# Kernel tuning notes

Measured on AMD Instinct MI355X. Metric: run time of the kernel, lower is better.

Reference implementation:

```python
import jax, jax.numpy as jnp
import numpy as np

ALPHA = 0.01  # leaky relu slope

def setup_inputs() -> dict:
    key = jax.random.key(0)
    ks = jax.random.split(key, 6)
    B, N1, N2, D_IN, D_OUT = 8, 2048, 2048, 256, 256
    return {
        "input_tensor1": jax.random.normal(ks[0], (B, N1, D_IN), jnp.float32),
        "attention_mask1": jnp.zeros((B, 1, N1), jnp.float32),
        "input_tensor2": jax.random.normal(ks[1], (B, N2, D_IN), jnp.float32),
        "attention_mask2": jnp.zeros((B, 1, N2), jnp.float32),
        "W1": jax.random.normal(ks[2], (D_IN, D_OUT), jnp.float32) * 0.05,
        "a1": jax.random.normal(ks[3], (2 * D_OUT, 1), jnp.float32) * 0.05,
        "W2": jax.random.normal(ks[4], (D_IN, D_OUT), jnp.float32) * 0.05,
        "a2": jax.random.normal(ks[5], (2 * D_OUT, 1), jnp.float32) * 0.05,
    }

def _cross_attn(Wh_q, Wh_k, a, mask):
    d = Wh_q.shape[-1]
    # additive GAT-style scores: [B, Nq, 1] + [B, 1, Nk] -> [B, Nq, Nk]
    s_q = Wh_q @ a[:d, :]            # [B, Nq, 1]
    s_k = Wh_k @ a[d:, :]            # [B, Nk, 1]
    e = s_q + jnp.swapaxes(s_k, -1, -2)
    e = jax.nn.leaky_relu(e, negative_slope=ALPHA)
    probs = jax.nn.softmax(e + mask, axis=-1)
    ctx = probs @ Wh_k               # [B, Nq, d]
    return ctx, probs

def reference(input_tensor1, attention_mask1, input_tensor2, attention_mask2, W1, a1, W2, a2):
    # dropout in eval mode (identity) for a deterministic reference
    Wh11 = input_tensor1 @ W1
    Wh12 = input_tensor2 @ W1
    ctx1, probs1 = _cross_attn(Wh11, Wh12, a1, attention_mask2)
    Wh22 = input_tensor2 @ W2
    Wh21 = input_tensor1 @ W2
    ctx2, probs2 = _cross_attn(Wh22, Wh21, a2, attention_mask1)
    return ctx1, ctx2, probs1, probs2
```

## Files before the change

kernel.cpp:

```cpp
#include <hip/hip_runtime.h>
#include <hip/hip_bf16.h>
#include <stdint.h>

#define ALPHA 0.01f

typedef __attribute__((ext_vector_type(8))) short short8;
typedef __attribute__((ext_vector_type(4))) float f32x4;
typedef __attribute__((ext_vector_type(4))) float float4_;
typedef __attribute__((ext_vector_type(4))) unsigned short ushort4_;
typedef unsigned int u32;

static __device__ __forceinline__ unsigned short f2bf(float f) {
    union { float f; u32 u; } v; v.f = f;
    u32 r = v.u + 0x7FFF + ((v.u >> 16) & 1);
    return (unsigned short)(r >> 16);
}

static __device__ __forceinline__ void lds_load16(const void* g, void* l) {
    __builtin_amdgcn_global_load_lds((const __attribute__((address_space(1))) u32*)g,
                                     (__attribute__((address_space(3))) u32*)l, 16, 0, 0);
}

__global__ __launch_bounds__(256) void k_prep(const float* __restrict__ W1, const float* __restrict__ a1,
                                              const float* __restrict__ W2, const float* __restrict__ a2,
                                              unsigned short* __restrict__ W1T, unsigned short* __restrict__ W2T,
                                              float* __restrict__ u) {
    int bb = blockIdx.x;
    if (bb < 512) {
        const float* W = (bb & 256) ? W2 : W1;
        unsigned short* WT = (bb & 256) ? W2T : W1T;
        int n = bb & 255, k = threadIdx.x;
        WT[n * 256 + k] = f2bf(W[k * 256 + n]);
    } else {
        int v = bb - 512;
        const float* W = (v < 2) ? W1 : W2;
        const float* a = ((v < 2) ? a1 : a2) + (v & 1) * 256;
        int d = threadIdx.x;
        float acc = 0.f;
        for (int n = 0; n < 256; n++) acc += W[d * 256 + n] * a[n];
        u[v * 256 + d] = acc;
    }
}

__global__ __launch_bounds__(256) void k_cast_s(const float* __restrict__ in1, const float* __restrict__ in2,
                                                const float* __restrict__ u,
                                                unsigned short* __restrict__ in1b, unsigned short* __restrict__ in2b,
                                                float* __restrict__ s) {
    int gid = blockIdx.x * 4 + (threadIdx.x >> 6);
    int tensor = gid >> 14;
    int row = gid & 16383;
    int lane = threadIdx.x & 63;
    const float* in = tensor ? in2 : in1;
    unsigned short* outb = tensor ? in2b : in1b;
    const float* uA = u + (tensor ? 256 : 0);
    const float* uB = u + (tensor ? 512 : 768);
    float* sA = s + (tensor ? 1 : 0) * 16384;
    float* sB = s + (tensor ? 2 : 3) * 16384;

    float4_ v = *(const float4_*)(in + row * 256 + lane * 4);
    float4_ ua = *(const float4_*)(uA + lane * 4);
    float4_ ub = *(const float4_*)(uB + lane * 4);
    ushort4_ ob;
    ob.x = f2bf(v.x); ob.y = f2bf(v.y); ob.z = f2bf(v.z); ob.w = f2bf(v.w);
    *(ushort4_*)(outb + row * 256 + lane * 4) = ob;
    float accA = v.x * ua.x + v.y * ua.y + v.z * ua.z + v.w * ua.w;
    float accB = v.x * ub.x + v.y * ub.y + v.z * ub.z + v.w * ub.w;
    for (int off = 32; off; off >>= 1) {
        accA += __shfl_xor(accA, off, 64);
        accB += __shfl_xor(accB, off, 64);
    }
    if (lane == 0) { sA[row] = accA; sB[row] = accB; }
}

__global__ __launch_bounds__(256) void k_gemm_whT(const unsigned short* __restrict__ W1T,
                                                  const unsigned short* __restrict__ W2T,
                                                  const unsigned short* __restrict__ in1b,
                                                  const unsigned short* __restrict__ in2b,
                                                  unsigned short* __restrict__ whT1,
                                                  unsigned short* __restrict__ whT2) {
    __shared__ __attribute__((aligned(16))) unsigned short sA[2][128 * 32];
    __shared__ __attribute__((aligned(16))) unsigned short sB[2][128 * 32];
    int c = blockIdx.x >> 8;
    int bid = blockIdx.x & 255;
    int mt = bid & 1, ntile = bid >> 1;
    const unsigned short* A = c ? W2T : W1T;
    const unsigned short* Bm = c ? in1b : in2b;
    unsigned short* outp = c ? whT2 : whT1;
    int t = threadIdx.x;
    int w = t >> 6, lane = t & 63, l15 = lane & 15, lq = lane >> 4;
    int wm = (w & 1) * 64, wn = (w >> 1) * 64;
    f32x4 acc[4][4] = {};
    const unsigned short* gA = A + (mt * 128 + (t >> 2)) * 256 + (t & 3) * 8;
    const unsigned short* gB = Bm + (ntile * 128 + (t >> 2)) * 256 + (t & 3) * 8;

    lds_load16(gA, &sA[0][t * 8]);
    lds_load16(gA + 64 * 256, &sA[0][t * 8 + 2048]);
    lds_load16(gB, &sB[0][t * 8]);
    lds_load16(gB + 64 * 256, &sB[0][t * 8 + 2048]);

    for (int it = 0; it < 8; ++it) {
        int kn = ((it + 1) & 7) * 32;
        unsigned short* dA = (unsigned short*)sA[(it + 1) & 1];
        unsigned short* dB = (unsigned short*)sB[(it + 1) & 1];
        lds_load16(gA + kn, dA + t * 8);
        lds_load16(gA + kn + 64 * 256, dA + t * 8 + 2048);
        lds_load16(gB + kn, dB + t * 8);
        lds_load16(gB + kn + 64 * 256, dB + t * 8 + 2048);
        __builtin_amdgcn_sched_barrier(0);
        asm volatile("s_waitcnt vmcnt(4)" ::: "memory");
        __builtin_amdgcn_s_barrier();

        const unsigned short* cA = sA[it & 1];
        const unsigned short* cB = sB[it & 1];
        short8 af[4], bfr[4];
#pragma unroll
        for (int m2 = 0; m2 < 4; m2++) af[m2] = *(const short8*)&cA[(wm + m2 * 16 + l15) * 32 + lq * 8];
#pragma unroll
        for (int n2 = 0; n2 < 4; n2++) bfr[n2] = *(const short8*)&cB[(wn + n2 * 16 + l15) * 32 + lq * 8];
        __builtin_amdgcn_s_setprio(1);
#pragma unroll
        for (int m2 = 0; m2 < 4; m2++)
#pragma unroll
            for (int n2 = 0; n2 < 4; n2++)
                acc[m2][n2] = __builtin_amdgcn_mfma_f32_16x16x32_bf16(af[m2], bfr[n2], acc[m2][n2], 0, 0, 0);
        __builtin_amdgcn_s_setprio(0);
        asm volatile("s_waitcnt lgkmcnt(0)" ::: "memory");
        __builtin_amdgcn_s_barrier();
    }
#pragma unroll
    for (int m2 = 0; m2 < 4; m2++) {
#pragma unroll
        for (int n2 = 0; n2 < 4; n2++) {
            int i_glob = ntile * 128 + wn + n2 * 16 + l15;
            int bb = i_glob >> 11, ii = i_glob & 2047;
#pragma unroll
            for (int r = 0; r < 4; r++) {
                int d = mt * 128 + wm + m2 * 16 + lq * 4 + r;
                outp[bb * (256 * 2048) + d * 2048 + ii] = f2bf(acc[m2][n2][r]);
            }
        }
    }
}

__global__ __launch_bounds__(512, 4) void k_attn(const float* __restrict__ s,
                                                 const unsigned short* __restrict__ whT1,
                                                 const unsigned short* __restrict__ whT2,
                                                 const float* __restrict__ mask1, const float* __restrict__ mask2,
                                                 float* __restrict__ out) {
    __shared__ __attribute__((aligned(16))) unsigned short sP[64 * 40];
    __shared__ __attribute__((aligned(16))) unsigned short sV[2][256 * 32];
    __shared__ float lsk[2048];
    __shared__ float lmk[2048];
    __shared__ float lsq[64], lmx[64], lil[64];
    __shared__ float red[16];

    int lb = (blockIdx.x & 7) * 64 + (blockIdx.x >> 3);
    int a = lb >> 8, b = (lb >> 5) & 7, rg = lb & 31;
    int t = threadIdx.x;
    const float* skp = s + (a ? 3 : 1) * 16384 + b * 2048;
    const float* sqp = s + (a ? 2 : 0) * 16384 + b * 2048 + rg * 64;
    const float* mp = (a ? mask1 : mask2) + b * 2048;
    const unsigned short* V = (a ? whT2 : whT1) + b * (256 * 2048);
    float* pout = out + 8388608 + a * 33554432 + (b * 2048 + rg * 64) * 2048;
    float* cout = out + a * 4194304 + (b * 2048 + rg * 64) * 256;

    float kmax = -3.4e38f, mmax = -3.4e38f;
    for (int j = t; j < 2048; j += 512) {
        float kv = skp[j], mv = mp[j];
        lsk[j] = kv; lmk[j] = mv;
        kmax = fmaxf(kmax, kv); mmax = fmaxf(mmax, mv);
    }
    if (t < 64) lsq[t] = sqp[t];
    int w = t >> 6, lane = t & 63;
    for (int off = 32; off; off >>= 1) {
        kmax = fmaxf(kmax, __shfl_xor(kmax, off, 64));
        mmax = fmaxf(mmax, __shfl_xor(mmax, off, 64));
    }
    if (lane == 0) { red[w] = kmax; red[8 + w] = mmax; }
    __syncthreads();
    float skmax = fmaxf(fmaxf(fmaxf(red[0], red[1]), fmaxf(red[2], red[3])),
                        fmaxf(fmaxf(red[4], red[5]), fmaxf(red[6], red[7])));
    float mkmax = fmaxf(fmaxf(fmaxf(red[8], red[9]), fmaxf(red[10], red[11])),
                        fmaxf(fmaxf(red[12], red[13]), fmaxf(red[14], red[15])));

    const float L2E = 1.44269504f;
    for (int rr = 0; rr < 8; rr++) {
        int row = w * 8 + rr;
        float sq = lsq[row];
        float mb = sq + skmax; mb = fmaxf(mb, mb * ALPHA) + mkmax;
        float mL2 = mb * L2E;
        float sum = 0.f;
        for (int j = lane; j < 2048; j += 64) {
            float x = sq + lsk[j];
            x = fmaxf(x, x * ALPHA) + lmk[j];
            sum += exp2f(__builtin_fmaf(x, L2E, -mL2));
        }
        for (int off = 32; off; off >>= 1) sum += __shfl_xor(sum, off, 64);
        if (lane == 0) { lmx[row] = mL2; lil[row] = 1.0f / sum; }
    }
    __syncthreads();

    int l15 = lane & 15, lq = lane >> 4;
    int wr = w >> 2, wc = w & 3;
    f32x4 acc[2][4] = {};
    int pi = t >> 3, pj = (t & 7) * 4;
    const unsigned short* gV = V + (t >> 2) * 2048 + (t & 3) * 8;
    float sqv = lsq[pi];
    float mL2 = lmx[pi], ilv = lil[pi];
    float* gp = pout + pi * 2048 + pj;
    const float* lskp = lsk + pj;
    const float* lmkp = lmk + pj;
    unsigned short* sPp = sP + pi * 40 + pj;

    lds_load16(gV, &sV[0][t * 8]);
    lds_load16(gV + 128 * 2048, &sV[0][t * 8 + 4096]);

    for (int it = 0; it < 64; ++it) {
        int j0 = it * 32;
        int jn = (j0 + 32) & 2047;
        unsigned short* dst = (unsigned short*)sV[(it + 1) & 1];
        lds_load16(gV + jn, dst + t * 8);
        lds_load16(gV + jn + 128 * 2048, dst + t * 8 + 4096);
        __builtin_amdgcn_sched_barrier(0);

        float pv[4];
#pragma unroll
        for (int q = 0; q < 4; q++) {
            float x = sqv + lskp[j0 + q];
            x = fmaxf(x, x * ALPHA) + lmkp[j0 + q];
            pv[q] = exp2f(__builtin_fmaf(x, L2E, -mL2)) * ilv;
        }
        float4_ v0; v0.x = pv[0]; v0.y = pv[1]; v0.z = pv[2]; v0.w = pv[3];
        __builtin_nontemporal_store(v0, (float4_*)(gp + j0));
        union { unsigned long long u64; unsigned short us[4]; } pk;
        pk.us[0] = f2bf(pv[0]); pk.us[1] = f2bf(pv[1]); pk.us[2] = f2bf(pv[2]); pk.us[3] = f2bf(pv[3]);
        *(unsigned long long*)sPp = pk.u64;

        asm volatile("s_waitcnt vmcnt(3) lgkmcnt(0)" ::: "memory");
        __builtin_amdgcn_s_barrier();

        const unsigned short* sVc = sV[it & 1];
        short8 af[2], bfr[4];
#pragma unroll
        for (int m2 = 0; m2 < 2; m2++) af[m2] = *(const short8*)&sP[(wr * 32 + m2 * 16 + l15) * 40 + lq * 8];
#pragma unroll
        for (int n2 = 0; n2 < 4; n2++) bfr[n2] = *(const short8*)&sVc[(wc * 64 + n2 * 16 + l15) * 32 + lq * 8];
        __builtin_amdgcn_s_setprio(1);
#pragma unroll
        for (int m2 = 0; m2 < 2; m2++)
#pragma unroll
            for (int n2 = 0; n2 < 4; n2++)
                acc[m2][n2] = __builtin_amdgcn_mfma_f32_16x16x32_bf16(af[m2], bfr[n2], acc[m2][n2], 0, 0, 0);
        __builtin_amdgcn_s_setprio(0);
        asm volatile("s_waitcnt lgkmcnt(0)" ::: "memory");
        __builtin_amdgcn_s_barrier();
    }

#pragma unroll
    for (int m2 = 0; m2 < 2; m2++) {
#pragma unroll
        for (int n2 = 0; n2 < 4; n2++) {
#pragma unroll
            for (int r = 0; r < 4; r++) {
                int i_loc = wr * 32 + m2 * 16 + lq * 4 + r;
                int d_loc = wc * 64 + n2 * 16 + l15;
                __builtin_nontemporal_store(acc[m2][n2][r], cout + i_loc * 256 + d_loc);
            }
        }
    }
}

extern "C" void kernel_launch(void* const* d_in, const int* in_sizes, int n_in,
                              void* d_out, int out_size, void* d_ws, size_t ws_size,
                              hipStream_t stream) {
    const float* in1   = (const float*)d_in[0];
    const float* mask1 = (const float*)d_in[1];
    const float* in2   = (const float*)d_in[2];
    const float* mask2 = (const float*)d_in[3];
    const float* W1    = (const float*)d_in[4];
    const float* a1    = (const float*)d_in[5];
    const float* W2    = (const float*)d_in[6];
    const float* a2    = (const float*)d_in[7];
    float* out = (float*)d_out;
    char* ws = (char*)d_ws;

    unsigned short* in1b = (unsigned short*)(ws);
    unsigned short* in2b = (unsigned short*)(ws + 8388608);
    unsigned short* whT1 = (unsigned short*)(ws + 16777216);
    unsigned short* whT2 = (unsigned short*)(ws + 25165824);
    unsigned short* W1T  = (unsigned short*)(ws + 33554432);
    unsigned short* W2T  = (unsigned short*)(ws + 33685504);
    float* u    = (float*)(ws + 33816576);
    float* s    = (float*)(ws + 33820672);

    k_prep<<<516, 256, 0, stream>>>(W1, a1, W2, a2, W1T, W2T, u);
    k_cast_s<<<8192, 256, 0, stream>>>(in1, in2, u, in1b, in2b, s);
    k_gemm_whT<<<512, 256, 0, stream>>>(W1T, W2T, in1b, in2b, whT1, whT2);
    k_attn<<<512, 512, 0, stream>>>(s, whT1, whT2, mask1, mask2, out);
}
```

Measured before the change: 404.9 us.

## Load V fragments directly to registers, double-buffer P with one barrier per step

The attention loop drops the LDS staging of V. Each wave now owns 32 output columns and reads its bf16 V fragments straight from global memory into registers. The step size grows from 32 to 64 keys, P is double-buffered in LDS so each iteration needs a single barrier instead of two, and log2(e) is folded into the scores up front so the leaky-relu/exp path uses fewer operations. This cuts LDS traffic and synchronisation, but V loads lose the async prefetch overlap and are no longer shared across waves through LDS.

```diff
diff --git a/kernel.cpp b/kernel.cpp
--- a/kernel.cpp
+++ b/kernel.cpp
@@ -147,10 +147,9 @@
                                                  const unsigned short* __restrict__ whT2,
                                                  const float* __restrict__ mask1, const float* __restrict__ mask2,
                                                  float* __restrict__ out) {
-    __shared__ __attribute__((aligned(16))) unsigned short sP[64 * 40];
-    __shared__ __attribute__((aligned(16))) unsigned short sV[2][256 * 32];
-    __shared__ float lsk[2048];
-    __shared__ float lmk[2048];
+    __shared__ __attribute__((aligned(16))) unsigned short sP[2][64 * 72];
+    __shared__ float lsk2[2048];
+    __shared__ float lmk2[2048];
     __shared__ float lsq[64], lmx[64], lil[64];
     __shared__ float red[16];
 
@@ -164,13 +163,14 @@
     float* pout = out + 8388608 + a * 33554432 + (b * 2048 + rg * 64) * 2048;
     float* cout = out + a * 4194304 + (b * 2048 + rg * 64) * 256;
 
+    const float L2E = 1.44269504f;
     float kmax = -3.4e38f, mmax = -3.4e38f;
     for (int j = t; j < 2048; j += 512) {
-        float kv = skp[j], mv = mp[j];
-        lsk[j] = kv; lmk[j] = mv;
+        float kv = skp[j] * L2E, mv = mp[j] * L2E;
+        lsk2[j] = kv; lmk2[j] = mv;
         kmax = fmaxf(kmax, kv); mmax = fmaxf(mmax, mv);
     }
-    if (t < 64) lsq[t] = sqp[t];
+    if (t < 64) lsq[t] = sqp[t] * L2E;
     int w = t >> 6, lane = t & 63;
     for (int off = 32; off; off >>= 1) {
         kmax = fmaxf(kmax, __shfl_xor(kmax, off, 64));
@@ -183,17 +183,19 @@
     float mkmax = fmaxf(fmaxf(fmaxf(red[8], red[9]), fmaxf(red[10], red[11])),
                         fmaxf(fmaxf(red[12], red[13]), fmaxf(red[14], red[15])));
 
-    const float L2E = 1.44269504f;
     for (int rr = 0; rr < 8; rr++) {
         int row = w * 8 + rr;
-        float sq = lsq[row];
-        float mb = sq + skmax; mb = fmaxf(mb, mb * ALPHA) + mkmax;
-        float mL2 = mb * L2E;
+        float sqL2 = lsq[row];
+        float yM = sqL2 + skmax;
+        float mL2 = fmaxf(yM, yM * ALPHA) + mkmax;
+        float cc = -mL2;
+        float sqc = sqL2 + cc;
+        float sq01 = __builtin_fmaf(ALPHA, sqL2, cc);
         float sum = 0.f;
         for (int j = lane; j < 2048; j += 64) {
-            float x = sq + lsk[j];
-            x = fmaxf(x, x * ALPHA) + lmk[j];
-            sum += exp2f(__builtin_fmaf(x, L2E, -mL2));
+            float k2 = lsk2[j];
+            float e = fmaxf(sqc + k2, __builtin_fmaf(ALPHA, k2, sq01)) + lmk2[j];
+            sum += exp2f(e);
         }
         for (int off = 32; off; off >>= 1) sum += __shfl_xor(sum, off, 64);
         if (lane == 0) { lmx[row] = mL2; lil[row] = 1.0f / sum; }
@@ -201,69 +203,69 @@
     __syncthreads();
 
     int l15 = lane & 15, lq = lane >> 4;
-    int wr = w >> 2, wc = w & 3;
-    f32x4 acc[2][4] = {};
-    int pi = t >> 3, pj = (t & 7) * 4;
-    const unsigned short* gV = V + (t >> 2) * 2048 + (t & 3) * 8;
-    float sqv = lsq[pi];
-    float mL2 = lmx[pi], ilv = lil[pi];
-    float* gp = pout + pi * 2048 + pj;
-    const float* lskp = lsk + pj;
-    const float* lmkp = lmk + pj;
-    unsigned short* sPp = sP + pi * 40 + pj;
-
-    lds_load16(gV, &sV[0][t * 8]);
-    lds_load16(gV + 128 * 2048, &sV[0][t * 8 + 4096]);
-
-    for (int it = 0; it < 64; ++it) {
-        int j0 = it * 32;
-        int jn = (j0 + 32) & 2047;
-        unsigned short* dst = (unsigned short*)sV[(it + 1) & 1];
-        lds_load16(gV + jn, dst + t * 8);
-        lds_load16(gV + jn + 128 * 2048, dst + t * 8 + 4096);
-        __builtin_amdgcn_sched_barrier(0);
-
-        float pv[4];
-#pragma unroll
-        for (int q = 0; q < 4; q++) {
-            float x = sqv + lskp[j0 + q];
-            x = fmaxf(x, x * ALPHA) + lmkp[j0 + q];
-            pv[q] = exp2f(__builtin_fmaf(x, L2E, -mL2)) * ilv;
+    f32x4 acc[4][2] = {};
+    int pi = t >> 3, pjq = t & 7;
+    float sqL2 = lsq[pi], ilv = lil[pi];
+    float cc = -lmx[pi];
+    float sqc = sqL2 + cc;
+    float sq01 = __builtin_fmaf(ALPHA, sqL2, cc);
+    const float* kkp = lsk2 + pjq * 8;
+    const float* mmp = lmk2 + pjq * 8;
+    float* gp = pout + pi * 2048 + pjq * 8;
+    const unsigned short* gV = V + (w * 32 + l15) * 2048 + lq * 8;
+
+    for (int it = 0; it < 32; ++it) {
+        int j0 = it * 64;
+        short8 bfr[2][2];
+#pragma unroll
+        for (int n2 = 0; n2 < 2; n2++)
+#pragma unroll
+            for (int ks = 0; ks < 2; ks++)
+                bfr[n2][ks] = *(const short8*)(gV + n2 * (16 * 2048) + j0 + ks * 32);
+
+        float pv[8];
+#pragma unroll
+        for (int q = 0; q < 8; q++) {
+            float k2 = kkp[j0 + q];
+            float e = fmaxf(sqc + k2, __builtin_fmaf(ALPHA, k2, sq01)) + mmp[j0 + q];
+            pv[q] = exp2f(e) * ilv;
         }
-        float4_ v0; v0.x = pv[0]; v0.y = pv[1]; v0.z = pv[2]; v0.w = pv[3];
+        float4_ v0, v1;
+        v0.x = pv[0]; v0.y = pv[1]; v0.z = pv[2]; v0.w = pv[3];
+        v1.x = pv[4]; v1.y = pv[5]; v1.z = pv[6]; v1.w = pv[7];
         __builtin_nontemporal_store(v0, (float4_*)(gp + j0));
-        union { unsigned long long u64; unsigned short us[4]; } pk;
-        pk.us[0] = f2bf(pv[0]); pk.us[1] = f2bf(pv[1]); pk.us[2] = f2bf(pv[2]); pk.us[3] = f2bf(pv[3]);
-        *(unsigned long long*)sPp = pk.u64;
-
-        asm volatile("s_waitcnt vmcnt(3) lgkmcnt(0)" ::: "memory");
-        __builtin_amdgcn_s_barrier();
-
-        const unsigned short* sVc = sV[it & 1];
-        short8 af[2], bfr[4];
-#pragma unroll
-        for (int m2 = 0; m2 < 2; m2++) af[m2] = *(const short8*)&sP[(wr * 32 + m2 * 16 + l15) * 40 + lq * 8];
-#pragma unroll
-        for (int n2 = 0; n2 < 4; n2++) bfr[n2] = *(const short8*)&sVc[(wc * 64 + n2 * 16 + l15) * 32 + lq * 8];
-        __builtin_amdgcn_s_setprio(1);
-#pragma unroll
-        for (int m2 = 0; m2 < 2; m2++)
-#pragma unroll
-            for (int n2 = 0; n2 < 4; n2++)
-                acc[m2][n2] = __builtin_amdgcn_mfma_f32_16x16x32_bf16(af[m2], bfr[n2], acc[m2][n2], 0, 0, 0);
-        __builtin_amdgcn_s_setprio(0);
+        __builtin_nontemporal_store(v1, (float4_*)(gp + j0) + 1);
+        union { short8 v; unsigned short us[8]; } pk;
+#pragma unroll
+        for (int q = 0; q < 8; q++) pk.us[q] = f2bf(pv[q]);
+        *(short8*)&sP[it & 1][pi * 72 + pjq * 8] = pk.v;
+
         asm volatile("s_waitcnt lgkmcnt(0)" ::: "memory");
         __builtin_amdgcn_s_barrier();
-    }
-
-#pragma unroll
-    for (int m2 = 0; m2 < 2; m2++) {
-#pragma unroll
-        for (int n2 = 0; n2 < 4; n2++) {
+        __builtin_amdgcn_sched_barrier(0);
+
+        const unsigned short* sp = sP[it & 1];
+        __builtin_amdgcn_s_setprio(1);
+#pragma unroll
+        for (int ks = 0; ks < 2; ks++)
+#pragma unroll
+            for (int m2 = 0; m2 < 4; m2++) {
+                short8 af = *(const short8*)&sp[(m2 * 16 + l15) * 72 + ks * 32 + lq * 8];
+#pragma unroll
+                for (int n2 = 0; n2 < 2; n2++)
+                    acc[m2][n2] = __builtin_amdgcn_mfma_f32_16x16x32_bf16(af, bfr[n2][ks], acc[m2][n2], 0, 0, 0);
+            }
+        __builtin_amdgcn_s_setprio(0);
+    }
+
+#pragma unroll
+    for (int m2 = 0; m2 < 4; m2++) {
+#pragma unroll
+        for (int n2 = 0; n2 < 2; n2++) {
 #pragma unroll
             for (int r = 0; r < 4; r++) {
-                int i_loc = wr * 32 + m2 * 16 + lq * 4 + r;
-                int d_loc = wc * 64 + n2 * 16 + l15;
+                int i_loc = m2 * 16 + lq * 4 + r;
+                int d_loc = w * 32 + n2 * 16 + l15;
                 __builtin_nontemporal_store(acc[m2][n2][r], cout + i_loc * 256 + d_loc);
             }
         }
```

Measured after the change: 430.5 us. +6.3%, slower.
